# Kernel tuning notes

Measured on AMD Instinct MI355X. Metric: run time of the kernel, lower is better.

## Reference

```python
import jax, jax.numpy as jnp
import numpy as np

B, S = 16, 512
IN_DIM, ATTN_DIM, DEPTH, HEADS, DH = 512, 512, 4, 8, 64
CB_DIM, CB_SIZE, MAX_SEQ = 64, 8192, 544


def _ln(x, g, b):
    mu = x.mean(-1, keepdims=True)
    v = ((x - mu) ** 2).mean(-1, keepdims=True)
    return (x - mu) / jnp.sqrt(v + 1e-5) * g + b


def setup_inputs() -> dict:
    key = jax.random.key(0)
    ks = jax.random.split(key, 16)
    sc = 0.02
    d = {
        "x": jax.random.normal(ks[0], (B, S, IN_DIM), jnp.float32),
        "w_in": jax.random.normal(ks[1], (IN_DIM, ATTN_DIM), jnp.float32) * sc,
        "b_in": jnp.zeros((ATTN_DIM,), jnp.float32),
        "pos_emb": jax.random.normal(ks[2], (MAX_SEQ, ATTN_DIM), jnp.float32) * sc,
        "ln1_g": jnp.ones((DEPTH, ATTN_DIM), jnp.float32),
        "ln1_b": jnp.zeros((DEPTH, ATTN_DIM), jnp.float32),
        "wq": jax.random.normal(ks[3], (DEPTH, ATTN_DIM, ATTN_DIM), jnp.float32) * sc,
        "wk": jax.random.normal(ks[4], (DEPTH, ATTN_DIM, ATTN_DIM), jnp.float32) * sc,
        "wv": jax.random.normal(ks[5], (DEPTH, ATTN_DIM, ATTN_DIM), jnp.float32) * sc,
        "wo": jax.random.normal(ks[6], (DEPTH, ATTN_DIM, ATTN_DIM), jnp.float32) * sc,
        "ln2_g": jnp.ones((DEPTH, ATTN_DIM), jnp.float32),
        "ln2_b": jnp.zeros((DEPTH, ATTN_DIM), jnp.float32),
        "ff_w1": jax.random.normal(ks[7], (DEPTH, ATTN_DIM, 4 * ATTN_DIM), jnp.float32) * sc,
        "ff_b1": jnp.zeros((DEPTH, 4 * ATTN_DIM), jnp.float32),
        "ff_w2": jax.random.normal(ks[8], (DEPTH, 4 * ATTN_DIM, ATTN_DIM), jnp.float32) * sc,
        "ff_b2": jnp.zeros((DEPTH, ATTN_DIM), jnp.float32),
        "lnf_g": jnp.ones((ATTN_DIM,), jnp.float32),
        "lnf_b": jnp.zeros((ATTN_DIM,), jnp.float32),
        "w_out": jax.random.normal(ks[9], (ATTN_DIM, CB_DIM), jnp.float32) * sc,
        "b_out": jnp.zeros((CB_DIM,), jnp.float32),
        "codebook": jax.random.normal(ks[10], (CB_SIZE, CB_DIM), jnp.float32),
    }
    return d


def _attn(h, wq, wk, wv, wo):
    b, s, _ = h.shape
    q = jnp.einsum('bsd,de->bse', h, wq).reshape(b, s, HEADS, DH)
    k = jnp.einsum('bsd,de->bse', h, wk).reshape(b, s, HEADS, DH)
    v = jnp.einsum('bsd,de->bse', h, wv).reshape(b, s, HEADS, DH)
    scores = jnp.einsum('bqhd,bkhd->bhqk', q, k) * (DH ** -0.5)
    a = jax.nn.softmax(scores, axis=-1)
    o = jnp.einsum('bhqk,bkhd->bqhd', a, v).reshape(b, s, ATTN_DIM)
    return jnp.einsum('bse,ed->bsd', o, wo)


def reference(x, w_in, b_in, pos_emb, ln1_g, ln1_b, wq, wk, wv, wo,
              ln2_g, ln2_b, ff_w1, ff_b1, ff_w2, ff_b2, lnf_g, lnf_b,
              w_out, b_out, codebook):
    s = x.shape[1]
    # ContinuousTransformerWrapper: project in + absolute pos emb
    h = jnp.einsum('bsd,de->bse', x, w_in) + b_in + pos_emb[:s]
    # pre-norm encoder layers: attn + ff, each residual
    for i in range(DEPTH):
        h = h + _attn(_ln(h, ln1_g[i], ln1_b[i]), wq[i], wk[i], wv[i], wo[i])
        g = _ln(h, ln2_g[i], ln2_b[i])
        g = jax.nn.gelu(jnp.einsum('bsd,df->bsf', g, ff_w1[i]) + ff_b1[i])
        h = h + jnp.einsum('bsf,fd->bsd', g, ff_w2[i]) + ff_b2[i]
    h = _ln(h, lnf_g, lnf_b)
    z = jnp.einsum('bsd,dc->bsc', h, w_out) + b_out  # [B,S,CB_DIM]
    # VectorQuantize: euclidean nearest codebook entry
    d2 = (z ** 2).sum(-1, keepdims=True) - 2.0 * jnp.einsum('bsc,kc->bsk', z, codebook) \
         + (codebook ** 2).sum(-1)  # [B,S,CB_SIZE]
    idx = jnp.argmin(d2, axis=-1)
    q = codebook[idx]  # [B,S,CB_DIM]
    commit_loss = jnp.mean((jax.lax.stop_gradient(q) - z) ** 2)  # commitment_weight=1.0
    q_st = z + jax.lax.stop_gradient(q - z)  # straight-through
    return q_st.sum(axis=1), commit_loss
```

## Files before the change

kernel.cpp:

```cpp
#include <hip/hip_runtime.h>
#include <cmath>

#define BATCH 16
#define SEQ 512
#define DMODEL 512
#define NDEPTH 4
#define NHEADS 8
#define DHEAD 64
#define DFF 2048
#define CBD 64
#define CBS 8192
#define MROWS (BATCH * SEQ)

typedef unsigned short u16;
typedef __attribute__((ext_vector_type(8))) short short8;
typedef __attribute__((ext_vector_type(4))) float f32x4;
typedef __attribute__((ext_vector_type(4))) unsigned short u16x4;

__device__ __forceinline__ u16 f2bf(float f) {
    unsigned u = __float_as_uint(f);
    u += 0x7fff + ((u >> 16) & 1);
    return (u16)(u >> 16);
}
__device__ __forceinline__ float bf2f(u16 h) {
    return __uint_as_float(((unsigned)h) << 16);
}

__device__ __forceinline__ void async16(u16* lds, const u16* g) {
    __builtin_amdgcn_global_load_lds(
        (const __attribute__((address_space(1))) unsigned int*)g,
        (__attribute__((address_space(3))) unsigned int*)lds, 16, 0, 0);
}

__device__ __forceinline__ float gelu_tanh(float u) {
    float t = fmaf(0.07135481627f * u, u * u, 1.5957691216f * u);
    return u / (1.0f + __expf(-t));
}

__global__ void zero_kernel(float* __restrict__ p, int n) {
    int i = blockIdx.x * 256 + threadIdx.x;
    if (i < n) p[i] = 0.0f;
}

__global__ void cbn_kernel(const float* __restrict__ cb, float* __restrict__ cbn) {
    int c = blockIdx.x * 256 + threadIdx.x;
    if (c >= CBS) return;
    const float* row = cb + (size_t)c * CBD;
    float s = 0.0f;
#pragma unroll
    for (int d = 0; d < CBD; ++d) s += row[d] * row[d];
    cbn[c] = s;
}

__global__ __launch_bounds__(256) void wtrans_kernel(
    const float* __restrict__ W, u16* __restrict__ Th, u16* __restrict__ Tl,
    int K, int N, long inLS, long outLS) {
    __shared__ float t[32][33];
    const float* Ws = W + (size_t)blockIdx.z * inLS;
    u16* Tho = Th + (size_t)blockIdx.z * outLS;
    u16* Tlo = Tl + (size_t)blockIdx.z * outLS;
    int n0 = blockIdx.x * 32, k0 = blockIdx.y * 32;
    int tx = threadIdx.x & 31, ty = threadIdx.x >> 5;
#pragma unroll
    for (int r = ty; r < 32; r += 8) t[r][tx] = Ws[(size_t)(k0 + r) * N + n0 + tx];
    __syncthreads();
#pragma unroll
    for (int r = ty; r < 32; r += 8) {
        float v = t[tx][r];
        size_t o = (size_t)(n0 + r) * K + k0 + tx;
        u16 hh = f2bf(v);
        Tho[o] = hh;
        Tlo[o] = f2bf(v - bf2f(hh));
    }
}

__global__ __launch_bounds__(256) void vtrans_kernel(
    const u16* __restrict__ Qh, const u16* __restrict__ Ql,
    u16* __restrict__ VTh, u16* __restrict__ VTl) {
    __shared__ u16 t[64][68];
    int s0 = blockIdx.x * 64;
    int hh = blockIdx.y;
    int b = blockIdx.z & 15, plane = blockIdx.z >> 4;
    const u16* src = (plane ? Ql : Qh) + ((size_t)(16 + hh) * MROWS) * 64;
    u16* dst = (plane ? VTl : VTh);
    int tid = threadIdx.x;
    int rr = tid >> 4, c4 = (tid & 15) * 4;
#pragma unroll
    for (int i = 0; i < 4; ++i) {
        int r = rr + i * 16;
        const u16* p = src + (size_t)(b * SEQ + s0 + r) * 64 + c4;
        *(u16x4*)(&t[r][c4]) = *(const u16x4*)p;
    }
    __syncthreads();
#pragma unroll
    for (int i = 0; i < 4; ++i) {
        int r = rr + i * 16;
        u16x4 v;
        v.x = t[c4 + 0][r]; v.y = t[c4 + 1][r]; v.z = t[c4 + 2][r]; v.w = t[c4 + 3][r];
        *(u16x4*)(dst + (size_t)b * SEQ * DMODEL + (size_t)(hh * 64 + r) * SEQ + s0 + c4) = v;
    }
}

__global__ void split_kernel(const float* __restrict__ X, u16* __restrict__ H,
                             u16* __restrict__ L, int n) {
    int i = blockIdx.x * 256 + threadIdx.x;
    if (i < n) {
        float v = X[i];
        u16 hh = f2bf(v);
        H[i] = hh;
        L[i] = f2bf(v - bf2f(hh));
    }
}

__global__ __launch_bounds__(256) void ln_kernel(
    const float* __restrict__ X,
    const float* __restrict__ C0, const float* __restrict__ C1,
    const float* __restrict__ bias2, const float* __restrict__ pos2,
    float* __restrict__ Xout,
    float* __restrict__ Y, u16* __restrict__ Yh, u16* __restrict__ Yl,
    const float* __restrict__ g, const float* __restrict__ b) {
    int row  = blockIdx.x * 4 + (threadIdx.x >> 6);
    int lane = threadIdx.x & 63;
    float v[8];
    float s = 0.0f;
#pragma unroll
    for (int j = 0; j < 8; ++j) {
        int d = lane + j * 64;
        size_t o = (size_t)row * DMODEL + d;
        float t = X ? X[o] : 0.0f;
        if (C0)    t += C0[o] + C1[o];
        if (bias2) t += bias2[d];
        if (pos2)  t += pos2[(size_t)(row & (SEQ - 1)) * DMODEL + d];
        v[j] = t;
        if (Xout) Xout[o] = t;
        s += t;
    }
#pragma unroll
    for (int off = 32; off; off >>= 1) s += __shfl_xor(s, off);
    float mu  = s * (1.0f / DMODEL);
    float var = 0.0f;
#pragma unroll
    for (int j = 0; j < 8; ++j) { float d = v[j] - mu; var += d * d; }
#pragma unroll
    for (int off = 32; off; off >>= 1) var += __shfl_xor(var, off);
    float r = rsqrtf(var * (1.0f / DMODEL) + 1e-5f);
#pragma unroll
    for (int j = 0; j < 8; ++j) {
        int d = lane + j * 64;
        float y = (v[j] - mu) * r * g[d] + b[d];
        size_t o = (size_t)row * DMODEL + d;
        if (Y) Y[o] = y;
        if (Yh) {
            u16 hh = f2bf(y);
            Yh[o] = hh;
            Yl[o] = f2bf(y - bf2f(hh));
        }
    }
}

__global__ __launch_bounds__(256) void gemm3_kernel(
    const u16* __restrict__ Ah, const u16* __restrict__ Al,
    const u16* __restrict__ Bh, const u16* __restrict__ Bl,
    float* __restrict__ Cf, u16* __restrict__ Ch, u16* __restrict__ Cl,
    const float* __restrict__ bias, const float* __restrict__ res,
    const float* __restrict__ pos, int M, int N, int K, int gelu,
    float* __restrict__ Cs0, float* __restrict__ Cs1, int kslice, int qkvscatter) {
    __shared__ __align__(16) u16 AsH[128 * 64];
    __shared__ __align__(16) u16 AsL[128 * 64];
    __shared__ __align__(16) u16 BsH[128 * 64];
    __shared__ __align__(16) u16 BsL[128 * 64];

    int tid  = threadIdx.x;
    int w    = tid >> 6, lane = tid & 63;
    int wr   = w >> 1, wc = w & 1;
    int quad = lane >> 4, l16 = lane & 15;
    int m0   = blockIdx.x * 128;
    int n0   = blockIdx.y * 128;
    int ksA  = (kslice > 0) ? blockIdx.z * kslice : 0;
    int ksB  = (kslice > 0) ? ksA + kslice : K;

    f32x4 acc[4][4];
#pragma unroll
    for (int i = 0; i < 4; ++i)
#pragma unroll
        for (int j = 0; j < 4; ++j) acc[i][j] = (f32x4){0.f, 0.f, 0.f, 0.f};

    int ldsoff[4];
    size_t goff[4];
#pragma unroll
    for (int r = 0; r < 4; ++r) {
        int cidx = tid + 256 * r;
        int row = cidx >> 3;
        int cg = (cidx & 7) ^ (row & 7);
        ldsoff[r] = cidx * 8;
        goff[r] = (size_t)row * K + cg * 8;
    }

    const u16* AbaseH = Ah + (size_t)m0 * K;
    const u16* AbaseL = Al + (size_t)m0 * K;
    const u16* BbaseH = Bh + (size_t)n0 * K;
    const u16* BbaseL = Bl + (size_t)n0 * K;

    for (int ks = ksA; ks < ksB; ks += 64) {
        __syncthreads();
#pragma unroll
        for (int r = 0; r < 4; ++r) {
            size_t g = goff[r] + ks;
            async16(&AsH[ldsoff[r]], AbaseH + g);
            async16(&AsL[ldsoff[r]], AbaseL + g);
            async16(&BsH[ldsoff[r]], BbaseH + g);
            async16(&BsL[ldsoff[r]], BbaseL + g);
        }
        __syncthreads();
#pragma unroll
        for (int s = 0; s < 2; ++s) {
            short8 afh[4], afl[4];
#pragma unroll
            for (int i = 0; i < 4; ++i) {
                int row = wr * 64 + i * 16 + l16;
                int off = row * 64 + (((s << 2) | quad) ^ (row & 7)) * 8;
                afh[i] = *(const short8*)&AsH[off];
                afl[i] = *(const short8*)&AsL[off];
            }
#pragma unroll
            for (int j = 0; j < 4; ++j) {
                int rowb = wc * 64 + j * 16 + l16;
                int offb = rowb * 64 + (((s << 2) | quad) ^ (rowb & 7)) * 8;
                short8 bh = *(const short8*)&BsH[offb];
                short8 bl = *(const short8*)&BsL[offb];
#pragma unroll
                for (int i = 0; i < 4; ++i) {
                    acc[i][j] = __builtin_amdgcn_mfma_f32_16x16x32_bf16(afh[i], bh, acc[i][j], 0, 0, 0);
                    acc[i][j] = __builtin_amdgcn_mfma_f32_16x16x32_bf16(afl[i], bh, acc[i][j], 0, 0, 0);
                    acc[i][j] = __builtin_amdgcn_mfma_f32_16x16x32_bf16(afh[i], bl, acc[i][j], 0, 0, 0);
                }
            }
        }
    }

    float* Cspl = (kslice > 0) ? (blockIdx.z ? Cs1 : Cs0) : nullptr;
    int mbase = m0 + wr * 64;
    int nbase = n0 + wc * 64;
#pragma unroll
    for (int mi = 0; mi < 4; ++mi)
#pragma unroll
        for (int ni = 0; ni < 4; ++ni) {
            f32x4 a = acc[mi][ni];
#pragma unroll
            for (int r = 0; r < 4; ++r) {
                int m = mbase + mi * 16 + quad * 4 + r;
                int n = nbase + ni * 16 + l16;
                float v = a[r];
                size_t o = qkvscatter
                    ? ((size_t)(n >> 6) * M + m) * 64 + (n & 63)
                    : (size_t)m * N + n;
                if (Cspl) { Cspl[o] = v; continue; }
                if (bias) v += bias[n];
                if (pos)  v += pos[(size_t)(m & (SEQ - 1)) * N + n];
                if (res)  v += res[(size_t)m * N + n];
                if (gelu) v = gelu_tanh(v);
                if (Cf) Cf[o] = v;
                if (Ch) {
                    u16 hh = f2bf(v);
                    Ch[o] = hh;
                    Cl[o] = f2bf(v - bf2f(hh));
                }
            }
        }
}

__global__ __launch_bounds__(256) void gemm_kernel(
    const float* __restrict__ A, const float* __restrict__ Bm,
    float* __restrict__ C, const float* __restrict__ bias,
    int M, int N, int K) {
    __shared__ float As[16][68];
    __shared__ float Bs[16][64];
    int tid = threadIdx.x;
    int tx = tid & 15, ty = tid >> 4;
    int a_m = tid >> 2, a_k = (tid & 3) * 4;
    int b_k = tid >> 4, b_n = (tid & 15) * 4;
    const float* Arow = A + (size_t)(blockIdx.x * 64 + a_m) * K;
    const float* Bcol = Bm + (size_t)blockIdx.y * 64 + b_n;
    float acc[4][4] = {};
    for (int k0 = 0; k0 < K; k0 += 16) {
        float4 av = *(const float4*)(Arow + k0 + a_k);
        float4 bv = *(const float4*)(Bcol + (size_t)(k0 + b_k) * N);
        __syncthreads();
        As[a_k + 0][a_m] = av.x; As[a_k + 1][a_m] = av.y;
        As[a_k + 2][a_m] = av.z; As[a_k + 3][a_m] = av.w;
        *(float4*)(&Bs[b_k][b_n]) = bv;
        __syncthreads();
#pragma unroll
        for (int kk = 0; kk < 16; ++kk) {
            float4 a4 = *(const float4*)(&As[kk][ty * 4]);
            float4 b4 = *(const float4*)(&Bs[kk][tx * 4]);
            float ar[4] = {a4.x, a4.y, a4.z, a4.w};
            float br[4] = {b4.x, b4.y, b4.z, b4.w};
#pragma unroll
            for (int i = 0; i < 4; ++i)
#pragma unroll
                for (int j = 0; j < 4; ++j) acc[i][j] = fmaf(ar[i], br[j], acc[i][j]);
        }
    }
    int m0 = blockIdx.x * 64 + ty * 4;
    int n0 = blockIdx.y * 64 + tx * 4;
#pragma unroll
    for (int i = 0; i < 4; ++i) {
        float vv[4];
#pragma unroll
        for (int j = 0; j < 4; ++j) {
            float t = acc[i][j];
            if (bias) t += bias[n0 + j];
            vv[j] = t;
        }
        *(float4*)(C + (size_t)(m0 + i) * N + n0) = make_float4(vv[0], vv[1], vv[2], vv[3]);
    }
}

__global__ __launch_bounds__(256) void attn_flash_kernel(
    const u16* __restrict__ QKh, const u16* __restrict__ QKl,
    const u16* __restrict__ VTh, const u16* __restrict__ VTl,
    u16* __restrict__ Oh, u16* __restrict__ Ol) {
    int bh = blockIdx.x & 127;
    int qt = blockIdx.x >> 7;
    int bb = bh >> 3, hh = bh & 7;

    __shared__ __align__(16) float Pw[4][16 * 68];
    __shared__ __align__(16) u16 KsH[64 * 64];
    __shared__ __align__(16) u16 KsL[64 * 64];
    __shared__ __align__(16) u16 VsH[64 * 64];
    __shared__ __align__(16) u16 VsL[64 * 64];

    int tid = threadIdx.x;
    int w = tid >> 6, lane = tid & 63;
    int quad = lane >> 4, l16 = lane & 15;
    int qtile = qt * 4 + w;
    float* P = Pw[w];

    const u16* qrh = QKh + ((size_t)hh * MROWS + bb * SEQ + qtile * 16 + l16) * 64 + quad * 8;
    const u16* qrl = QKl + ((size_t)hh * MROWS + bb * SEQ + qtile * 16 + l16) * 64 + quad * 8;
    short8 Qh0 = *(const short8*)qrh;
    short8 Qh1 = *(const short8*)(qrh + 32);
    short8 Ql0 = *(const short8*)qrl;
    short8 Ql1 = *(const short8*)(qrl + 32);

    float lsum[4] = {0.f, 0.f, 0.f, 0.f};
    f32x4 acc[4];
#pragma unroll
    for (int dt = 0; dt < 4; ++dt) acc[dt] = (f32x4){0.f, 0.f, 0.f, 0.f};

    const u16* KbH = QKh + ((size_t)(8 + hh) * MROWS + bb * SEQ) * 64;
    const u16* KbL = QKl + ((size_t)(8 + hh) * MROWS + bb * SEQ) * 64;
    const u16* VbH = VTh + (size_t)bb * SEQ * DMODEL + (size_t)(hh * 64) * SEQ;
    const u16* VbL = VTl + (size_t)bb * SEQ * DMODEL + (size_t)(hh * 64) * SEQ;

    int ldsoff[2];
    int goffK[2];
    size_t goffV[2];
#pragma unroll
    for (int r = 0; r < 2; ++r) {
        int cidx = tid + 256 * r;
        int row = cidx >> 3;
        int cg = (cidx & 7) ^ (row & 7);
        ldsoff[r] = cidx * 8;
        goffK[r] = row * 64 + cg * 8;
        goffV[r] = (size_t)row * SEQ + cg * 8;
    }

    for (int kt = 0; kt < 8; ++kt) {
        int kb = kt * 64;
        __syncthreads();
#pragma unroll
        for (int r = 0; r < 2; ++r) {
            async16(&KsH[ldsoff[r]], KbH + (size_t)kb * 64 + goffK[r]);
            async16(&KsL[ldsoff[r]], KbL + (size_t)kb * 64 + goffK[r]);
            async16(&VsH[ldsoff[r]], VbH + kb + goffV[r]);
            async16(&VsL[ldsoff[r]], VbL + kb + goffV[r]);
        }
        __syncthreads();

#pragma unroll
        for (int s = 0; s < 4; ++s) {
            int row = s * 16 + l16;
            int c0 = (quad ^ (row & 7)) * 8;
            int c1 = ((quad | 4) ^ (row & 7)) * 8;
            f32x4 a = (f32x4){0.f, 0.f, 0.f, 0.f};
            {
                short8 Kh0 = *(const short8*)&KsH[row * 64 + c0];
                short8 Kh1 = *(const short8*)&KsH[row * 64 + c1];
                a = __builtin_amdgcn_mfma_f32_16x16x32_bf16(Qh0, Kh0, a, 0, 0, 0);
                a = __builtin_amdgcn_mfma_f32_16x16x32_bf16(Qh1, Kh1, a, 0, 0, 0);
                a = __builtin_amdgcn_mfma_f32_16x16x32_bf16(Ql0, Kh0, a, 0, 0, 0);
                a = __builtin_amdgcn_mfma_f32_16x16x32_bf16(Ql1, Kh1, a, 0, 0, 0);
            }
            {
                short8 Kl0 = *(const short8*)&KsL[row * 64 + c0];
                short8 Kl1 = *(const short8*)&KsL[row * 64 + c1];
                a = __builtin_amdgcn_mfma_f32_16x16x32_bf16(Qh0, Kl0, a, 0, 0, 0);
                a = __builtin_amdgcn_mfma_f32_16x16x32_bf16(Qh1, Kl1, a, 0, 0, 0);
            }
#pragma unroll
            for (int r = 0; r < 4; ++r) {
                float p = __expf(a[r] * 0.125f);
                lsum[r] += p;
                P[(quad * 4 + r) * 68 + s * 16 + l16] = p;
            }
        }
#pragma unroll
        for (int ks = 0; ks < 2; ++ks) {
            short8 ph, pl;
            {
                const float* src = &P[l16 * 68 + ks * 32 + quad * 8];
                f32x4 a0 = *(const f32x4*)src;
                f32x4 a1 = *(const f32x4*)(src + 4);
                float v[8] = {a0[0], a0[1], a0[2], a0[3], a1[0], a1[1], a1[2], a1[3]};
#pragma unroll
                for (int j = 0; j < 8; ++j) {
                    u16 hv = f2bf(v[j]);
                    ph[j] = (short)hv;
                    pl[j] = (short)f2bf(v[j] - bf2f(hv));
                }
            }
#pragma unroll
            for (int dt = 0; dt < 4; ++dt) {
                int rowv = dt * 16 + l16;
                int cv = (((ks << 2) | quad) ^ (rowv & 7)) * 8;
                short8 Vh = *(const short8*)&VsH[rowv * 64 + cv];
                short8 Vl = *(const short8*)&VsL[rowv * 64 + cv];
                acc[dt] = __builtin_amdgcn_mfma_f32_16x16x32_bf16(ph, Vh, acc[dt], 0, 0, 0);
                acc[dt] = __builtin_amdgcn_mfma_f32_16x16x32_bf16(pl, Vh, acc[dt], 0, 0, 0);
                acc[dt] = __builtin_amdgcn_mfma_f32_16x16x32_bf16(ph, Vl, acc[dt], 0, 0, 0);
            }
        }
    }

#pragma unroll
    for (int r = 0; r < 4; ++r) {
#pragma unroll
        for (int off = 8; off; off >>= 1) lsum[r] += __shfl_xor(lsum[r], off);
    }
#pragma unroll
    for (int r = 0; r < 4; ++r) {
        float inv = 1.0f / lsum[r];
        size_t rowoff = (size_t)(bb * SEQ + qtile * 16 + quad * 4 + r) * DMODEL + hh * 64;
#pragma unroll
        for (int dt = 0; dt < 4; ++dt) {
            float v = acc[dt][r] * inv;
            u16 hv = f2bf(v);
            Oh[rowoff + dt * 16 + l16] = hv;
            Ol[rowoff + dt * 16 + l16] = f2bf(v - bf2f(hv));
        }
    }
}

__global__ __launch_bounds__(256) void vq3_kernel(
    const float* __restrict__ Z, const u16* __restrict__ Zh, const u16* __restrict__ Zl,
    const u16* __restrict__ CBh, const u16* __restrict__ CBl,
    const float* __restrict__ CB, const float* __restrict__ CBN,
    float* __restrict__ out) {
    __shared__ float sbest[4][16];
    __shared__ int sidx[4][16];
    __shared__ int ibest[16];
    __shared__ float psum[4][64];
    __shared__ float cl4[4];

    int tid = threadIdx.x;
    int w = tid >> 6, lane = tid & 63;
    int quad = lane >> 4, l16 = lane & 15;
    int row0 = blockIdx.x * 16;

    const u16* zph = Zh + (size_t)(row0 + l16) * CBD + quad * 8;
    const u16* zpl = Zl + (size_t)(row0 + l16) * CBD + quad * 8;
    short8 Z0h = *(const short8*)zph;
    short8 Z1h = *(const short8*)(zph + 32);
    short8 Z0l = *(const short8*)zpl;
    short8 Z1l = *(const short8*)(zpl + 32);

    float best[4] = {3.4e38f, 3.4e38f, 3.4e38f, 3.4e38f};
    int bidx[4] = {0, 0, 0, 0};

    short8 A0h, A1h, A0l, A1l;  float An;
    short8 B0h, B1h, B0l, B1l;  float Bn;
    short8 C0h, C1h, C0l, C1l;  float Cn;
    short8 D0h, D1h, D0l, D1l;  float Dn;

#define LOADB(bk, cc) {                                            \
    int c_ = (cc);                                                 \
    const u16* ph_ = CBh + (size_t)c_ * CBD + quad * 8;            \
    const u16* pl_ = CBl + (size_t)c_ * CBD + quad * 8;            \
    bk##0h = *(const short8*)ph_;  bk##1h = *(const short8*)(ph_ + 32); \
    bk##0l = *(const short8*)pl_;  bk##1l = *(const short8*)(pl_ + 32); \
    bk##n  = CBN[c_]; }

#define COMPB(bk, cc) {                                                          \
    f32x4 a_ = (f32x4){0.f, 0.f, 0.f, 0.f};                                      \
    int c_ = (cc);                                                               \
    a_ = __builtin_amdgcn_mfma_f32_16x16x32_bf16(Z0h, bk##0h, a_, 0, 0, 0);      \
    a_ = __builtin_amdgcn_mfma_f32_16x16x32_bf16(Z1h, bk##1h, a_, 0, 0, 0);      \
    a_ = __builtin_amdgcn_mfma_f32_16x16x32_bf16(Z0l, bk##0h, a_, 0, 0, 0);      \
    a_ = __builtin_amdgcn_mfma_f32_16x16x32_bf16(Z1l, bk##1h, a_, 0, 0, 0);      \
    a_ = __builtin_amdgcn_mfma_f32_16x16x32_bf16(Z0h, bk##0l, a_, 0, 0, 0);      \
    a_ = __builtin_amdgcn_mfma_f32_16x16x32_bf16(Z1h, bk##1l, a_, 0, 0, 0);      \
    _Pragma("unroll")                                                            \
    for (int r = 0; r < 4; ++r) {                                                \
        float s_ = bk##n - 2.0f * a_[r];                                         \
        if (s_ < best[r]) { best[r] = s_; bidx[r] = c_; }                        \
    } }

    const int NW = CBS / 4;
    int cbase = w * NW;
    LOADB(A, cbase + l16);
    LOADB(B, cbase + 16 + l16);
    LOADB(C, cbase + 32 + l16);
    LOADB(D, cbase + 48 + l16);
    for (int t = 0; t < NW; t += 64) {
        COMPB(A, cbase + t + l16);       LOADB(A, cbase + ((t + 64)  & (NW - 1)) + l16);
        COMPB(B, cbase + t + 16 + l16);  LOADB(B, cbase + ((t + 80)  & (NW - 1)) + l16);
        COMPB(C, cbase + t + 32 + l16);  LOADB(C, cbase + ((t + 96)  & (NW - 1)) + l16);
        COMPB(D, cbase + t + 48 + l16);  LOADB(D, cbase + ((t + 112) & (NW - 1)) + l16);
    }

#undef LOADB
#undef COMPB

#pragma unroll
    for (int off = 8; off; off >>= 1) {
#pragma unroll
        for (int r = 0; r < 4; ++r) {
            float ov = __shfl_xor(best[r], off);
            int oi = __shfl_xor(bidx[r], off);
            if (ov < best[r] || (ov == best[r] && oi < bidx[r])) { best[r] = ov; bidx[r] = oi; }
        }
    }
    if (l16 == 0) {
#pragma unroll
        for (int r = 0; r < 4; ++r) {
            sbest[w][quad * 4 + r] = best[r];
            sidx[w][quad * 4 + r] = bidx[r];
        }
    }
    __syncthreads();
    if (tid < 16) {
        float bv = sbest[0][tid];
        int bi = sidx[0][tid];
#pragma unroll
        for (int ww = 1; ww < 4; ++ww) {
            float ov = sbest[ww][tid];
            int oi = sidx[ww][tid];
            if (ov < bv || (ov == bv && oi < bi)) { bv = ov; bi = oi; }
        }
        ibest[tid] = bi;
    }
    __syncthreads();

    int d2 = lane;
    float qacc = 0.0f, closs = 0.0f;
#pragma unroll
    for (int j = 0; j < 4; ++j) {
        int r2 = w * 4 + j;
        int bi = ibest[r2];
        float q = CB[(size_t)bi * CBD + d2];
        float z = Z[(size_t)(row0 + r2) * CBD + d2];
        qacc += q;
        float df = q - z;
        closs += df * df;
    }
    psum[w][d2] = qacc;
#pragma unroll
    for (int off = 32; off; off >>= 1) closs += __shfl_xor(closs, off);
    if (d2 == 0) cl4[w] = closs;
    __syncthreads();
    if (tid < 64) {
        float t = psum[0][tid] + psum[1][tid] + psum[2][tid] + psum[3][tid];
        int b = row0 >> 9;
        atomicAdd(out + b * 64 + tid, t);
    }
    if (tid == 0)
        atomicAdd(out + 1024, (cl4[0] + cl4[1] + cl4[2] + cl4[3]) * (1.0f / (float)(MROWS * CBD)));
}

extern "C" void kernel_launch(void* const* d_in, const int* in_sizes, int n_in,
                              void* d_out, int out_size, void* d_ws, size_t ws_size,
                              hipStream_t stream) {
    const float* x    = (const float*)d_in[0];
    const float* w_in = (const float*)d_in[1];
    const float* b_in = (const float*)d_in[2];
    const float* pos  = (const float*)d_in[3];
    const float* ln1g = (const float*)d_in[4];
    const float* ln1b = (const float*)d_in[5];
    const float* wq   = (const float*)d_in[6];
    const float* wk   = (const float*)d_in[7];
    const float* wv   = (const float*)d_in[8];
    const float* wo   = (const float*)d_in[9];
    const float* ln2g = (const float*)d_in[10];
    const float* ln2b = (const float*)d_in[11];
    const float* ffw1 = (const float*)d_in[12];
    const float* ffb1 = (const float*)d_in[13];
    const float* ffw2 = (const float*)d_in[14];
    const float* ffb2 = (const float*)d_in[15];
    const float* lnfg = (const float*)d_in[16];
    const float* lnfb = (const float*)d_in[17];
    const float* wout = (const float*)d_in[18];
    const float* bout = (const float*)d_in[19];
    const float* cb   = (const float*)d_in[20];
    float* out = (float*)d_out;

    const size_t MD  = (size_t)MROWS * DMODEL;
    const size_t MQ  = (size_t)MROWS * 1536;
    const size_t MF  = (size_t)MROWS * DFF;

    float* ws   = (float*)d_ws;
    float* h    = ws;
    float* t0   = h + MD;
    float* big  = t0 + MD;
    float* zb   = big + MF;
    float* cbn  = zb + (size_t)MROWS * CBD;
    u16* cbh    = (u16*)(cbn + CBS);
    u16* cbl    = cbh + (size_t)CBS * CBD;
    u16* t0h    = (u16*)(cbh + 2 * (size_t)CBS * CBD);
    u16* t0l    = t0h + MD;
    u16* wb     = t0l + MD;

    u16* qkvh = (u16*)big;
    u16* qkvl = qkvh + MQ;
    u16* obh  = qkvl + MQ;
    u16* obl  = obh + MD;
    u16* xh   = obh;
    u16* xl   = obl;
    u16* fmh  = (u16*)big;
    u16* fml  = fmh + MF;
    u16* zbh  = (u16*)big;
    u16* zbl  = zbh + (size_t)MROWS * CBD;

    const size_t S_WIN  = (size_t)DMODEL * DMODEL;
    const size_t S_QKV  = (size_t)1536 * DMODEL * NDEPTH;
    const size_t S_WO   = S_WIN * NDEPTH;
    const size_t S_FF1  = (size_t)DFF * DMODEL * NDEPTH;
    const size_t S_FF2  = S_FF1;
    u16* winT_h = wb;
    u16* winT_l = winT_h + S_WIN;
    u16* qkvT_h = winT_l + S_WIN;
    u16* qkvT_l = qkvT_h + S_QKV;
    u16* woT_h  = qkvT_l + S_QKV;
    u16* woT_l  = woT_h + S_WO;
    u16* ff1T_h = woT_l + S_WO;
    u16* ff1T_l = ff1T_h + S_FF1;
    u16* ff2T_h = ff1T_l + S_FF1;
    u16* ff2T_l = ff2T_h + S_FF2;
    u16* VTh = ff2T_l + S_FF2;
    u16* VTl = VTh + (size_t)BATCH * SEQ * DMODEL;
    float* spK0 = (float*)(VTl + (size_t)BATCH * SEQ * DMODEL);
    float* spK1 = spK0 + MD;

    dim3 blk(256);

    zero_kernel<<<dim3((out_size + 255) / 256), blk, 0, stream>>>(out, out_size);
    cbn_kernel<<<dim3(CBS / 256), blk, 0, stream>>>(cb, cbn);
    split_kernel<<<dim3((int)(CBS * CBD / 256)), blk, 0, stream>>>(cb, cbh, cbl, CBS * CBD);

    wtrans_kernel<<<dim3(16, 16, 1), blk, 0, stream>>>(w_in, winT_h, winT_l, DMODEL, DMODEL, 0, 0);
    wtrans_kernel<<<dim3(16, 16, NDEPTH), blk, 0, stream>>>(
        wq, qkvT_h, qkvT_l, DMODEL, DMODEL, (long)DMODEL * DMODEL, (long)1536 * DMODEL);
    wtrans_kernel<<<dim3(16, 16, NDEPTH), blk, 0, stream>>>(
        wk, qkvT_h + (size_t)512 * DMODEL, qkvT_l + (size_t)512 * DMODEL,
        DMODEL, DMODEL, (long)DMODEL * DMODEL, (long)1536 * DMODEL);
    wtrans_kernel<<<dim3(16, 16, NDEPTH), blk, 0, stream>>>(
        wv, qkvT_h + (size_t)1024 * DMODEL, qkvT_l + (size_t)1024 * DMODEL,
        DMODEL, DMODEL, (long)DMODEL * DMODEL, (long)1536 * DMODEL);
    wtrans_kernel<<<dim3(16, 16, NDEPTH), blk, 0, stream>>>(
        wo, woT_h, woT_l, DMODEL, DMODEL, (long)DMODEL * DMODEL, (long)DMODEL * DMODEL);
    wtrans_kernel<<<dim3(DFF / 32, 16, NDEPTH), blk, 0, stream>>>(
        ffw1, ff1T_h, ff1T_l, DMODEL, DFF, (long)DMODEL * DFF, (long)DFF * DMODEL);
    wtrans_kernel<<<dim3(16, DFF / 32, NDEPTH), blk, 0, stream>>>(
        ffw2, ff2T_h, ff2T_l, DFF, DMODEL, (long)DFF * DMODEL, (long)DMODEL * DFF);

    split_kernel<<<dim3((int)(MD / 256)), blk, 0, stream>>>(x, xh, xl, (int)MD);

    gemm3_kernel<<<dim3(MROWS / 128, DMODEL / 128, 2), blk, 0, stream>>>(
        xh, xl, winT_h, winT_l, nullptr, nullptr, nullptr, nullptr, nullptr, nullptr,
        MROWS, DMODEL, DMODEL, 0, spK0, spK1, 256, 0);

    for (int l = 0; l < NDEPTH; ++l) {
        ln_kernel<<<dim3(MROWS / 4), blk, 0, stream>>>(
            (l == 0) ? nullptr : h, spK0, spK1,
            (l == 0) ? b_in : (ffb2 + (size_t)(l - 1) * DMODEL),
            (l == 0) ? pos : nullptr, h,
            nullptr, t0h, t0l, ln1g + l * DMODEL, ln1b + l * DMODEL);
        gemm3_kernel<<<dim3(MROWS / 128, 1536 / 128, 1), blk, 0, stream>>>(
            t0h, t0l, qkvT_h + (size_t)l * 1536 * DMODEL, qkvT_l + (size_t)l * 1536 * DMODEL,
            nullptr, qkvh, qkvl, nullptr, nullptr, nullptr, MROWS, 1536, DMODEL, 0,
            nullptr, nullptr, 0, 1);
        vtrans_kernel<<<dim3(8, 8, 32), blk, 0, stream>>>(qkvh, qkvl, VTh, VTl);
        attn_flash_kernel<<<dim3(1024), blk, 0, stream>>>(
            qkvh, qkvl, VTh, VTl, obh, obl);
        gemm3_kernel<<<dim3(MROWS / 128, DMODEL / 128, 2), blk, 0, stream>>>(
            obh, obl, woT_h + (size_t)l * S_WIN, woT_l + (size_t)l * S_WIN,
            nullptr, nullptr, nullptr, nullptr, nullptr, nullptr,
            MROWS, DMODEL, DMODEL, 0, spK0, spK1, 256, 0);
        ln_kernel<<<dim3(MROWS / 4), blk, 0, stream>>>(
            h, spK0, spK1, nullptr, nullptr, h,
            nullptr, t0h, t0l, ln2g + l * DMODEL, ln2b + l * DMODEL);
        gemm3_kernel<<<dim3(MROWS / 128, DFF / 128, 1), blk, 0, stream>>>(
            t0h, t0l, ff1T_h + (size_t)l * DFF * DMODEL, ff1T_l + (size_t)l * DFF * DMODEL,
            nullptr, fmh, fml, ffb1 + l * DFF, nullptr, nullptr, MROWS, DFF, DMODEL, 1,
            nullptr, nullptr, 0, 0);
        gemm3_kernel<<<dim3(MROWS / 128, DMODEL / 128, 2), blk, 0, stream>>>(
            fmh, fml, ff2T_h + (size_t)l * DFF * DMODEL, ff2T_l + (size_t)l * DFF * DMODEL,
            nullptr, nullptr, nullptr, nullptr, nullptr, nullptr,
            MROWS, DMODEL, DFF, 0, spK0, spK1, 1024, 0);
    }

    ln_kernel<<<dim3(MROWS / 4), blk, 0, stream>>>(
        h, spK0, spK1, ffb2 + (size_t)3 * DMODEL, nullptr, nullptr,
        t0, nullptr, nullptr, lnfg, lnfb);
    gemm_kernel<<<dim3(MROWS / 64, 1), blk, 0, stream>>>(t0, wout, zb, bout, MROWS, CBD, DMODEL);
    split_kernel<<<dim3((int)((size_t)MROWS * CBD / 256)), blk, 0, stream>>>(
        zb, zbh, zbl, MROWS * CBD);
    vq3_kernel<<<dim3(MROWS / 16), blk, 0, stream>>>(zb, zbh, zbl, cbh, cbl, cb, cbn, out);
}
```

Measured before the change: 1.514 ms.

## Stage codebook tiles in swizzled LDS via async copies in VQ kernel

The VQ argmin kernel previously had each wave stream its own quarter of the codebook straight from global memory into registers, with four-deep software prefetching. Now all four waves cooperatively copy 64-code tiles of the hi/lo codebook into XOR-swizzled shared memory with async 16-byte loads, then read MFMA operands from LDS. This drops the per-wave global traffic, but it adds two block barriers per 64-code tile and removes the register-level prefetch overlap, so load latency is no longer hidden.

```diff
diff --git a/kernel.cpp b/kernel.cpp
--- a/kernel.cpp
+++ b/kernel.cpp
@@ -463,6 +463,8 @@
     __shared__ int ibest[16];
     __shared__ float psum[4][64];
     __shared__ float cl4[4];
+    __shared__ __align__(16) u16 CsH[64 * 64];
+    __shared__ __align__(16) u16 CsL[64 * 64];
 
     int tid = threadIdx.x;
     int w = tid >> 6, lane = tid & 63;
@@ -479,49 +481,48 @@
     float best[4] = {3.4e38f, 3.4e38f, 3.4e38f, 3.4e38f};
     int bidx[4] = {0, 0, 0, 0};
 
-    short8 A0h, A1h, A0l, A1l;  float An;
-    short8 B0h, B1h, B0l, B1l;  float Bn;
-    short8 C0h, C1h, C0l, C1l;  float Cn;
-    short8 D0h, D1h, D0l, D1l;  float Dn;
-
-#define LOADB(bk, cc) {                                            \
-    int c_ = (cc);                                                 \
-    const u16* ph_ = CBh + (size_t)c_ * CBD + quad * 8;            \
-    const u16* pl_ = CBl + (size_t)c_ * CBD + quad * 8;            \
-    bk##0h = *(const short8*)ph_;  bk##1h = *(const short8*)(ph_ + 32); \
-    bk##0l = *(const short8*)pl_;  bk##1l = *(const short8*)(pl_ + 32); \
-    bk##n  = CBN[c_]; }
-
-#define COMPB(bk, cc) {                                                          \
-    f32x4 a_ = (f32x4){0.f, 0.f, 0.f, 0.f};                                      \
-    int c_ = (cc);                                                               \
-    a_ = __builtin_amdgcn_mfma_f32_16x16x32_bf16(Z0h, bk##0h, a_, 0, 0, 0);      \
-    a_ = __builtin_amdgcn_mfma_f32_16x16x32_bf16(Z1h, bk##1h, a_, 0, 0, 0);      \
-    a_ = __builtin_amdgcn_mfma_f32_16x16x32_bf16(Z0l, bk##0h, a_, 0, 0, 0);      \
-    a_ = __builtin_amdgcn_mfma_f32_16x16x32_bf16(Z1l, bk##1h, a_, 0, 0, 0);      \
-    a_ = __builtin_amdgcn_mfma_f32_16x16x32_bf16(Z0h, bk##0l, a_, 0, 0, 0);      \
-    a_ = __builtin_amdgcn_mfma_f32_16x16x32_bf16(Z1h, bk##1l, a_, 0, 0, 0);      \
-    _Pragma("unroll")                                                            \
-    for (int r = 0; r < 4; ++r) {                                                \
-        float s_ = bk##n - 2.0f * a_[r];                                         \
-        if (s_ < best[r]) { best[r] = s_; bidx[r] = c_; }                        \
-    } }
-
-    const int NW = CBS / 4;
-    int cbase = w * NW;
-    LOADB(A, cbase + l16);
-    LOADB(B, cbase + 16 + l16);
-    LOADB(C, cbase + 32 + l16);
-    LOADB(D, cbase + 48 + l16);
-    for (int t = 0; t < NW; t += 64) {
-        COMPB(A, cbase + t + l16);       LOADB(A, cbase + ((t + 64)  & (NW - 1)) + l16);
-        COMPB(B, cbase + t + 16 + l16);  LOADB(B, cbase + ((t + 80)  & (NW - 1)) + l16);
-        COMPB(C, cbase + t + 32 + l16);  LOADB(C, cbase + ((t + 96)  & (NW - 1)) + l16);
-        COMPB(D, cbase + t + 48 + l16);  LOADB(D, cbase + ((t + 112) & (NW - 1)) + l16);
-    }
-
-#undef LOADB
-#undef COMPB
+    int ldsoff[2], goffC[2];
+#pragma unroll
+    for (int r = 0; r < 2; ++r) {
+        int cidx = tid + 256 * r;
+        int row = cidx >> 3;
+        int cg = (cidx & 7) ^ (row & 7);
+        ldsoff[r] = cidx * 8;
+        goffC[r] = row * 64 + cg * 8;
+    }
+
+    int rowc = w * 16 + l16;
+    int c0 = (quad ^ (rowc & 7)) * 8;
+    int c1 = ((quad | 4) ^ (rowc & 7)) * 8;
+
+    for (int t = 0; t < CBS; t += 64) {
+        __syncthreads();
+#pragma unroll
+        for (int r = 0; r < 2; ++r) {
+            async16(&CsH[ldsoff[r]], CBh + (size_t)t * 64 + goffC[r]);
+            async16(&CsL[ldsoff[r]], CBl + (size_t)t * 64 + goffC[r]);
+        }
+        __syncthreads();
+
+        int code = t + rowc;
+        short8 C0h = *(const short8*)&CsH[rowc * 64 + c0];
+        short8 C1h = *(const short8*)&CsH[rowc * 64 + c1];
+        short8 C0l = *(const short8*)&CsL[rowc * 64 + c0];
+        short8 C1l = *(const short8*)&CsL[rowc * 64 + c1];
+        float cn = CBN[code];
+        f32x4 a = (f32x4){0.f, 0.f, 0.f, 0.f};
+        a = __builtin_amdgcn_mfma_f32_16x16x32_bf16(Z0h, C0h, a, 0, 0, 0);
+        a = __builtin_amdgcn_mfma_f32_16x16x32_bf16(Z1h, C1h, a, 0, 0, 0);
+        a = __builtin_amdgcn_mfma_f32_16x16x32_bf16(Z0l, C0h, a, 0, 0, 0);
+        a = __builtin_amdgcn_mfma_f32_16x16x32_bf16(Z1l, C1h, a, 0, 0, 0);
+        a = __builtin_amdgcn_mfma_f32_16x16x32_bf16(Z0h, C0l, a, 0, 0, 0);
+        a = __builtin_amdgcn_mfma_f32_16x16x32_bf16(Z1h, C1l, a, 0, 0, 0);
+#pragma unroll
+        for (int r = 0; r < 4; ++r) {
+            float s = cn - 2.0f * a[r];
+            if (s < best[r]) { best[r] = s; bidx[r] = code; }
+        }
+    }
 
 #pragma unroll
     for (int off = 8; off; off >>= 1) {
```

After: 1.481 ms. -2.2%, faster.
